# Performance work log

Measured on AMD Instinct MI355X. Metric: run time of the kernel, lower is better.

The kernel has to match this reference:

```python
import jax, jax.numpy as jnp
import numpy as np

NUM_CLASSES = 256
WEIGHT = 0.0005
EPS = 1e-12  # torch F.normalize eps


def setup_inputs() -> dict:
    key = jax.random.key(0)
    k1, k2 = jax.random.split(key)
    features = jax.random.normal(k1, (32768, 1024), dtype=jnp.float32)
    labels = jax.random.randint(k2, (32768,), 0, NUM_CLASSES, dtype=jnp.int32)
    return {"features": features, "labels": labels}


def _centroid_loss(features, labels):
    B, D = features.shape
    # row-wise L2 normalize (torch F.normalize: x / max(||x||, eps))
    norms = jnp.linalg.norm(features, axis=1, keepdims=True)
    f = features / jnp.maximum(norms, EPS)

    ones = jnp.ones((B,), f.dtype)
    counts = jax.ops.segment_sum(ones, labels, num_segments=NUM_CLASSES)  # [C]
    sums = jax.ops.segment_sum(f, labels, num_segments=NUM_CLASSES)       # [C, D]

    # rank of each sample within its class (order of first appearance),
    # matching the row order of features[class_mask] in the original loop
    onehot = jax.nn.one_hot(labels, NUM_CLASSES, dtype=jnp.int32)          # [B, C]
    rank = jnp.take_along_axis(jnp.cumsum(onehot, axis=0), labels[:, None].astype(jnp.int32), axis=1)[:, 0] - 1

    # idx_table[c, r] = global index of the r-th member of class c; sentinel B if none
    idx_table = jnp.full((NUM_CLASSES, B), B, dtype=jnp.int32)
    idx_table = idx_table.at[labels, rank].set(jnp.arange(B, dtype=jnp.int32))

    # NOTE: the original code indexes class_features with the GLOBAL index i
    # (arange(n_c) != i), i.e. it excludes the member of the class at position i,
    # and excludes nothing when i >= n_c. We reproduce that exactly.
    arange_b = jnp.arange(B)
    k = idx_table[labels, arange_b]            # class member at in-class position i (global i)
    valid_excl = k < B                          # exclusion only happens when i < class size
    excl_feat = jnp.where(valid_excl[:, None], f[jnp.where(valid_excl, k, 0)], 0.0)

    n_c = counts[labels]                        # class size per sample (float)
    denom = jnp.where(valid_excl, n_c - 1.0, n_c)
    denom = jnp.maximum(denom, 1.0)             # safe for masked-out singleton classes
    centroid = (sums[labels] - excl_feat) / denom[:, None]

    dist = jnp.mean((f - centroid) ** 2, axis=1)  # F.mse_loss(..., reduction='mean')
    contrib = jnp.where(n_c > 1.0, dist, 0.0)     # skip classes with <=1 sample
    return WEIGHT * jnp.sum(contrib) / B


def reference(features, labels):
    return _centroid_loss(features, labels)
```

## Files before the change

### kernel.cpp

```cpp
#include <hip/hip_runtime.h>

#define BN 32768
#define DN 1024
#define CN 256
#define RCAP 320

__device__ __forceinline__ float dot4(float4 a, float4 b) {
    return a.x*b.x + a.y*b.y + a.z*b.z + a.w*b.w;
}

__global__ void __launch_bounds__(1024) k_all(const float4* __restrict__ x4,
                                              const int* __restrict__ labels,
                                              float* __restrict__ out) {
    __shared__ unsigned int packed[BN / 4];
    __shared__ unsigned long long smask[BN / 64];
    __shared__ int sic[RCAP];
    __shared__ float rnl[RCAP];
    __shared__ int wcnt[16];
    __shared__ float fa[(DN / 4) * 5];
    __shared__ float wred[4];
    __shared__ float dacc_s;

    const int c = blockIdx.x;
    const int t = threadIdx.x;

    for (int w = t; w < BN / 4; w += 1024) {
        const int4 v = ((const int4*)labels)[w];
        packed[w] = (unsigned int)(v.x & 255)
                  | ((unsigned int)(v.y & 255) << 8)
                  | ((unsigned int)(v.z & 255) << 16)
                  | ((unsigned int)(v.w & 255) << 24);
    }
    for (int i = t; i < (DN / 4) * 5; i += 1024) fa[i] = 0.0f;
    if (t == 0) dacc_s = 0.0f;
    __syncthreads();

    const int wave = t >> 6, lane = t & 63;
    const unsigned long long lt = (lane == 0) ? 0ull : (~0ull >> (64 - lane));
    const int ch0 = wave * 32, ch1 = ch0 + 32;

    int cnt = 0;
    for (int ch = ch0; ch < ch1; ++ch) {
        const int gi = ch * 64 + lane;
        const int lab = (packed[gi >> 2] >> ((gi & 3) * 8)) & 255;
        const unsigned long long mask = __ballot(lab == c);
        if (lane == 0) smask[ch] = mask;
        cnt += __popcll(mask);
    }
    if (lane == 0) wcnt[wave] = cnt;
    __syncthreads();

    int base = 0, ntot = 0;
    for (int w2 = 0; w2 < 16; ++w2) {
        const int v = wcnt[w2];
        if (w2 < wave) base += v;
        ntot += v;
    }

    for (int ch = ch0; ch < ch1; ++ch) {
        const unsigned long long mask = smask[ch];
        if ((mask >> lane) & 1ull) {
            const int pos = base + __popcll(mask & lt);
            if (pos < RCAP) sic[pos] = ch * 64 + lane;
        }
        base += __popcll(mask);
    }
    __syncthreads();

    const int nn = min(ntot, RCAP);
    float4 a0 = make_float4(0.f, 0.f, 0.f, 0.f), a1 = a0, a2 = a0, a3 = a0;
    for (int r = wave; r < nn; r += 16) {
        const int row = sic[r];
        const float4* b4 = x4 + (size_t)row * 256;
        const float4 v0 = b4[lane];
        const float4 v1 = b4[lane + 64];
        const float4 v2 = b4[lane + 128];
        const float4 v3 = b4[lane + 192];
        float ss = dot4(v0, v0) + dot4(v1, v1) + dot4(v2, v2) + dot4(v3, v3);
#pragma unroll
        for (int off = 32; off; off >>= 1) ss += __shfl_xor(ss, off, 64);
        const float rn = 1.0f / fmaxf(sqrtf(ss), 1e-12f);
        if (lane == 0) rnl[r] = rn;
        a0.x += v0.x * rn; a0.y += v0.y * rn; a0.z += v0.z * rn; a0.w += v0.w * rn;
        a1.x += v1.x * rn; a1.y += v1.y * rn; a1.z += v1.z * rn; a1.w += v1.w * rn;
        a2.x += v2.x * rn; a2.y += v2.y * rn; a2.z += v2.z * rn; a2.w += v2.w * rn;
        a3.x += v3.x * rn; a3.y += v3.y * rn; a3.z += v3.z * rn; a3.w += v3.w * rn;
    }

    {
        const int q0 = lane, q1 = lane + 64, q2 = lane + 128, q3 = lane + 192;
        atomicAdd(&fa[5 * q0 + 0], a0.x); atomicAdd(&fa[5 * q0 + 1], a0.y);
        atomicAdd(&fa[5 * q0 + 2], a0.z); atomicAdd(&fa[5 * q0 + 3], a0.w);
        atomicAdd(&fa[5 * q1 + 0], a1.x); atomicAdd(&fa[5 * q1 + 1], a1.y);
        atomicAdd(&fa[5 * q1 + 2], a1.z); atomicAdd(&fa[5 * q1 + 3], a1.w);
        atomicAdd(&fa[5 * q2 + 0], a2.x); atomicAdd(&fa[5 * q2 + 1], a2.y);
        atomicAdd(&fa[5 * q2 + 2], a2.z); atomicAdd(&fa[5 * q2 + 3], a2.w);
        atomicAdd(&fa[5 * q3 + 0], a3.x); atomicAdd(&fa[5 * q3 + 1], a3.y);
        atomicAdd(&fa[5 * q3 + 2], a3.z); atomicAdd(&fa[5 * q3 + 3], a3.w);
    }
    __syncthreads();

    float d = 0.0f;
    if (t < 256) {
        float4 Sq;
        Sq.x = fa[5 * t + 0]; Sq.y = fa[5 * t + 1];
        Sq.z = fa[5 * t + 2]; Sq.w = fa[5 * t + 3];
        d = dot4(Sq, Sq);
    }
    if (wave < 4) {
#pragma unroll
        for (int off = 32; off; off >>= 1) d += __shfl_xor(d, off, 64);
        if (lane == 0) wred[wave] = d;
    }
    __syncthreads();

    const int n = ntot;
    if (n >= 2) {
        const float s2 = wred[0] + wred[1] + wred[2] + wred[3];
        const int nlim = min(n, nn);

        for (int p = wave; p < nn; p += 16) {
            const int j = sic[p];
            if (j >= nlim) continue;
            const int k = sic[j];
            const float4* bi = x4 + (size_t)j * 256;
            const float4* bk = x4 + (size_t)k * 256;
            const float4 xi0 = bi[lane], xi1 = bi[lane + 64],
                         xi2 = bi[lane + 128], xi3 = bi[lane + 192];
            const float4 xk0 = bk[lane], xk1 = bk[lane + 64],
                         xk2 = bk[lane + 128], xk3 = bk[lane + 192];
            float4 S0, S1, S2, S3;
            {
                const int q0 = lane, q1 = lane + 64, q2 = lane + 128, q3 = lane + 192;
                S0.x = fa[5*q0+0]; S0.y = fa[5*q0+1]; S0.z = fa[5*q0+2]; S0.w = fa[5*q0+3];
                S1.x = fa[5*q1+0]; S1.y = fa[5*q1+1]; S1.z = fa[5*q1+2]; S1.w = fa[5*q1+3];
                S2.x = fa[5*q2+0]; S2.y = fa[5*q2+1]; S2.z = fa[5*q2+2]; S2.w = fa[5*q2+3];
                S3.x = fa[5*q3+0]; S3.y = fa[5*q3+1]; S3.z = fa[5*q3+2]; S3.w = fa[5*q3+3];
            }
            float d0 = dot4(xi0, S0) + dot4(xi1, S1) + dot4(xi2, S2) + dot4(xi3, S3);
            float d1 = dot4(xi0, xk0) + dot4(xi1, xk1) + dot4(xi2, xk2) + dot4(xi3, xk3);
            float d2 = dot4(xk0, S0) + dot4(xk1, S1) + dot4(xk2, S2) + dot4(xk3, S3);
            float d3 = dot4(xk0, xk0) + dot4(xk1, xk1) + dot4(xk2, xk2) + dot4(xk3, xk3);
#pragma unroll
            for (int off = 32; off; off >>= 1) {
                d0 += __shfl_xor(d0, off, 64);
                d1 += __shfl_xor(d1, off, 64);
                d2 += __shfl_xor(d2, off, 64);
                d3 += __shfl_xor(d3, off, 64);
            }
            if (lane == 0) {
                const float rni = rnl[p];
                const float rnk = rnl[j];
                const float fiS  = rni * d0;
                const float fifk = rni * rnk * d1;
                const float Sfk  = rnk * d2;
                const float fk2  = rnk * rnk * d3;
                const float nf = (float)n;
                const float dd = nf - 1.0f;
                const float naive = -2.0f * fiS / nf + s2 / (nf * nf);
                const float corr  = -2.0f * (fiS - fifk) / dd
                                  + (s2 - 2.0f * Sfk + fk2) / (dd * dd);
                atomicAdd(&dacc_s, corr - naive);
            }
        }
        __syncthreads();
        if (t == 0) {
            const float nf = (float)n;
            const float total = (nf - s2 / nf) + dacc_s;
            atomicAdd(out, total * (1.0f / DN) * (0.0005f / (float)BN));
        }
    }
}

extern "C" void kernel_launch(void* const* d_in, const int* in_sizes, int n_in,
                              void* d_out, int out_size, void* d_ws, size_t ws_size,
                              hipStream_t stream) {
    const float4* x4 = (const float4*)d_in[0];
    const int* labels = (const int*)d_in[1];
    float* out = (float*)d_out;

    hipMemsetAsync(out, 0, sizeof(float), stream);
    k_all<<<CN, 1024, 0, stream>>>(x4, labels, out);
}
```

Baseline: 219.5 us.

## Split centroid loss into norm, streaming class-sum, and finish kernels

Replaces the single per-class kernel with three kernels. A separate pass computes row inverse norms. A streaming kernel then accumulates per-class sums over row chunks and feature slices in shared memory and writes partials to workspace. The finish kernel reduces those partials per class and does the correction terms. This replaces the scattered per-class row gathers and the low-parallelism per-class summation with coalesced streaming. In exchange it reads the features twice, adds a 32MB partials round trip, and relies on heavy shared-memory atomics. It falls back to the old kernel if the workspace is too small.

Measured after the change: 377.0 us. 1.72x slower.

```diff
diff --git a/kernel.cpp b/kernel.cpp
--- a/kernel.cpp
+++ b/kernel.cpp
@@ -4,9 +4,207 @@
 #define DN 1024
 #define CN 256
 #define RCAP 320
+#define NCH 32
+#define CHR (BN/NCH)
+#define NSL 8
+#define SLF (DN/NSL)
 
 __device__ __forceinline__ float dot4(float4 a, float4 b) {
     return a.x*b.x + a.y*b.y + a.z*b.z + a.w*b.w;
+}
+
+
+__global__ void __launch_bounds__(256) k_norm(const float4* __restrict__ x4,
+                                              float* __restrict__ rnorm) {
+    const int lane = threadIdx.x & 63;
+    const int gw = (int)((blockIdx.x * 256u + threadIdx.x) >> 6);
+    for (int row = gw; row < BN; row += 8192) {
+        const float4* b4 = x4 + (size_t)row * 256;
+        const float4 v0 = b4[lane];
+        const float4 v1 = b4[lane + 64];
+        const float4 v2 = b4[lane + 128];
+        const float4 v3 = b4[lane + 192];
+        float ss = dot4(v0, v0) + dot4(v1, v1) + dot4(v2, v2) + dot4(v3, v3);
+#pragma unroll
+        for (int off = 32; off; off >>= 1) ss += __shfl_xor(ss, off, 64);
+        if (lane == 0) rnorm[row] = 1.0f / fmaxf(sqrtf(ss), 1e-12f);
+    }
+}
+
+__global__ void __launch_bounds__(1024) k_stream(const float* __restrict__ xf,
+                                                 const int* __restrict__ labels,
+                                                 const float* __restrict__ rnorm,
+                                                 float* __restrict__ partial) {
+    __shared__ float acc[CN][SLF];
+    __shared__ unsigned char slab[CHR];
+    __shared__ float rnv[CHR];
+
+    const int bid = blockIdx.x;
+    const int slice = bid & (NSL - 1);
+    const int chunk = bid >> 3;
+    const int t = threadIdx.x;
+
+    for (int i = t; i < CN * SLF; i += 1024) ((float*)acc)[i] = 0.0f;
+    if (t < CHR / 4) {
+        const int4 lv = ((const int4*)(labels + chunk * CHR))[t];
+        ((uchar4*)slab)[t] = make_uchar4((unsigned char)lv.x, (unsigned char)lv.y,
+                                         (unsigned char)lv.z, (unsigned char)lv.w);
+        ((float4*)rnv)[t] = ((const float4*)(rnorm + chunk * CHR))[t];
+    }
+    __syncthreads();
+
+    const int wave = t >> 6, lane = t & 63;
+    const int half = lane >> 5, cl = lane & 31;
+
+    for (int it = 0; it < CHR / 32; ++it) {
+        const int rloc = it * 32 + wave * 2 + half;
+        const float* base = xf + (size_t)(chunk * CHR + rloc) * DN + slice * SLF;
+        const float v0 = base[cl];
+        const float v1 = base[cl + 32];
+        const float v2 = base[cl + 64];
+        const float v3 = base[cl + 96];
+        const float rn = rnv[rloc];
+        const int lab = slab[rloc];
+        atomicAdd(&acc[lab][cl],      v0 * rn);
+        atomicAdd(&acc[lab][cl + 32], v1 * rn);
+        atomicAdd(&acc[lab][cl + 64], v2 * rn);
+        atomicAdd(&acc[lab][cl + 96], v3 * rn);
+    }
+    __syncthreads();
+
+    for (int u = t; u < CN * (SLF / 4); u += 1024) {
+        const int cls = u >> 5, q = u & 31;
+        ((float4*)partial)[((size_t)chunk * CN + cls) * (DN / 4) + slice * (SLF / 4) + q]
+            = ((const float4*)acc[cls])[q];
+    }
+}
+
+__global__ void __launch_bounds__(1024) k_finish(const float4* __restrict__ x4,
+                                                 const int* __restrict__ labels,
+                                                 const float* __restrict__ rnorm,
+                                                 const float* __restrict__ partial,
+                                                 float* __restrict__ out) {
+    __shared__ unsigned int packed[BN / 4];
+    __shared__ unsigned long long smask[BN / 64];
+    __shared__ int sic[RCAP];
+    __shared__ float rnl[RCAP];
+    __shared__ int wcnt[16];
+    __shared__ float Sl[DN];
+    __shared__ float wred[16];
+    __shared__ float dacc_s;
+
+    const int c = blockIdx.x;
+    const int t = threadIdx.x;
+    const int wave = t >> 6, lane = t & 63;
+
+    for (int w = t; w < BN / 4; w += 1024) {
+        const int4 v = ((const int4*)labels)[w];
+        packed[w] = (unsigned int)(v.x & 255)
+                  | ((unsigned int)(v.y & 255) << 8)
+                  | ((unsigned int)(v.z & 255) << 16)
+                  | ((unsigned int)(v.w & 255) << 24);
+    }
+    if (t == 0) dacc_s = 0.0f;
+
+    float Sv = 0.0f;
+    for (int ch = 0; ch < NCH; ++ch)
+        Sv += partial[((size_t)ch * CN + c) * DN + t];
+    Sl[t] = Sv;
+
+    float dsq = Sv * Sv;
+#pragma unroll
+    for (int off = 32; off; off >>= 1) dsq += __shfl_xor(dsq, off, 64);
+    if (lane == 0) wred[wave] = dsq;
+    __syncthreads();
+
+    const unsigned long long lt = (lane == 0) ? 0ull : (~0ull >> (64 - lane));
+    const int ch0 = wave * 32, ch1 = ch0 + 32;
+
+    int cnt = 0;
+    for (int ch = ch0; ch < ch1; ++ch) {
+        const int gi = ch * 64 + lane;
+        const int lab = (packed[gi >> 2] >> ((gi & 3) * 8)) & 255;
+        const unsigned long long mask = __ballot(lab == c);
+        if (lane == 0) smask[ch] = mask;
+        cnt += __popcll(mask);
+    }
+    if (lane == 0) wcnt[wave] = cnt;
+    __syncthreads();
+
+    int base = 0, ntot = 0;
+    for (int w2 = 0; w2 < 16; ++w2) {
+        const int v = wcnt[w2];
+        if (w2 < wave) base += v;
+        ntot += v;
+    }
+
+    for (int ch = ch0; ch < ch1; ++ch) {
+        const unsigned long long mask = smask[ch];
+        if ((mask >> lane) & 1ull) {
+            const int pos = base + __popcll(mask & lt);
+            if (pos < RCAP) {
+                const int gi = ch * 64 + lane;
+                sic[pos] = gi;
+                rnl[pos] = rnorm[gi];
+            }
+        }
+        base += __popcll(mask);
+    }
+    __syncthreads();
+
+    const int n = ntot;
+    if (n >= 2) {
+        float s2 = 0.0f;
+        for (int w2 = 0; w2 < 16; ++w2) s2 += wred[w2];
+        const int nn = min(n, RCAP);
+        const int nlim = nn;
+
+        const float4* Sl4 = (const float4*)Sl;
+        for (int p = wave; p < nn; p += 16) {
+            const int j = sic[p];
+            if (j >= nlim) continue;
+            const int k = sic[j];
+            const float4* bi = x4 + (size_t)j * 256;
+            const float4* bk = x4 + (size_t)k * 256;
+            const float4 xi0 = bi[lane], xi1 = bi[lane + 64],
+                         xi2 = bi[lane + 128], xi3 = bi[lane + 192];
+            const float4 xk0 = bk[lane], xk1 = bk[lane + 64],
+                         xk2 = bk[lane + 128], xk3 = bk[lane + 192];
+            const float4 S0 = Sl4[lane], S1 = Sl4[lane + 64],
+                         S2 = Sl4[lane + 128], S3 = Sl4[lane + 192];
+            float d0 = dot4(xi0, S0) + dot4(xi1, S1) + dot4(xi2, S2) + dot4(xi3, S3);
+            float d1 = dot4(xi0, xk0) + dot4(xi1, xk1) + dot4(xi2, xk2) + dot4(xi3, xk3);
+            float d2 = dot4(xk0, S0) + dot4(xk1, S1) + dot4(xk2, S2) + dot4(xk3, S3);
+            float d3 = dot4(xk0, xk0) + dot4(xk1, xk1) + dot4(xk2, xk2) + dot4(xk3, xk3);
+#pragma unroll
+            for (int off = 32; off; off >>= 1) {
+                d0 += __shfl_xor(d0, off, 64);
+                d1 += __shfl_xor(d1, off, 64);
+                d2 += __shfl_xor(d2, off, 64);
+                d3 += __shfl_xor(d3, off, 64);
+            }
+            if (lane == 0) {
+                const float rni = rnl[p];
+                const float rnk = rnl[j];
+                const float fiS  = rni * d0;
+                const float fifk = rni * rnk * d1;
+                const float Sfk  = rnk * d2;
+                const float fk2  = rnk * rnk * d3;
+                const float nf = (float)n;
+                const float dd = nf - 1.0f;
+                const float naive = -2.0f * fiS / nf + s2 / (nf * nf);
+                const float corr  = -2.0f * (fiS - fifk) / dd
+                                  + (s2 - 2.0f * Sfk + fk2) / (dd * dd);
+                atomicAdd(&dacc_s, corr - naive);
+            }
+        }
+        __syncthreads();
+        if (t == 0) {
+            const float nf = (float)n;
+            const float total = (nf - s2 / nf) + dacc_s;
+            atomicAdd(out, total * (1.0f / DN) * (0.0005f / (float)BN));
+        }
+    }
 }
 
 __global__ void __launch_bounds__(1024) k_all(const float4* __restrict__ x4,
@@ -118,7 +316,6 @@
     if (n >= 2) {
         const float s2 = wred[0] + wred[1] + wred[2] + wred[3];
         const int nlim = min(n, nn);
-
         for (int p = wave; p < nn; p += 16) {
             const int j = sic[p];
             if (j >= nlim) continue;
@@ -176,9 +373,22 @@
                               void* d_out, int out_size, void* d_ws, size_t ws_size,
                               hipStream_t stream) {
     const float4* x4 = (const float4*)d_in[0];
+    const float* xf = (const float*)d_in[0];
     const int* labels = (const int*)d_in[1];
     float* out = (float*)d_out;
+    char* ws = (char*)d_ws;
+
+    const size_t P_OFF = 131072;
+    const size_t NEED = P_OFF + (size_t)NCH * CN * DN * 4;
 
     hipMemsetAsync(out, 0, sizeof(float), stream);
-    k_all<<<CN, 1024, 0, stream>>>(x4, labels, out);
-}
+    if (ws_size >= NEED) {
+        float* rnorm = (float*)ws;
+        float* partial = (float*)(ws + P_OFF);
+        k_norm<<<2048, 256, 0, stream>>>(x4, rnorm);
+        k_stream<<<NCH * NSL, 1024, 0, stream>>>(xf, labels, rnorm, partial);
+        k_finish<<<CN, 1024, 0, stream>>>(x4, labels, rnorm, partial, out);
+    } else {
+        k_all<<<CN, 1024, 0, stream>>>(x4, labels, out);
+    }
+}
```
